# Optimization experiments

Hardware: AMD Instinct MI355X
Metric: run time of the kernel (lower is better)

The kernel has to match this reference:

```python
import jax, jax.numpy as jnp
import numpy as np

B, T, C = 8, 1024, 768
NH = 12
HD = C // NH  # 64


def setup_inputs() -> dict:
    key = jax.random.key(0)
    k1, k2, k3 = jax.random.split(key, 3)
    x = jax.random.normal(k1, (B, T, C), dtype=jnp.float32)
    w_attn = jax.random.normal(k2, (C, 3 * C), dtype=jnp.float32) * 0.02
    b_attn = jnp.zeros((3 * C,), dtype=jnp.float32)
    w_proj = jax.random.normal(k3, (C, C), dtype=jnp.float32) * 0.02
    b_proj = jnp.zeros((C,), dtype=jnp.float32)
    return {"x": x, "w_attn": w_attn, "b_attn": b_attn, "w_proj": w_proj, "b_proj": b_proj}


def reference(x, w_attn, b_attn, w_proj, b_proj):
    Bb, Tt, Cc = x.shape
    qkv = x @ w_attn + b_attn  # [B,T,3C]
    q, k, v = jnp.split(qkv, [Cc, 2 * Cc], axis=-1)
    # [B, NH, T, HD]
    q = q.reshape(Bb, Tt, NH, HD).swapaxes(1, 2)
    k = k.reshape(Bb, Tt, NH, HD).swapaxes(1, 2)
    v = v.reshape(Bb, Tt, NH, HD).swapaxes(1, 2)
    scale = 1.0 / jnp.sqrt(jnp.asarray(HD, dtype=x.dtype))
    att = jnp.einsum("bhqd,bhkd->bhqk", q, k) * scale  # [B,NH,T,T]
    causal = jnp.tril(jnp.ones((Tt, Tt), dtype=bool))[None, None]
    att = jnp.where(causal, att, jnp.asarray(-jnp.inf, dtype=att.dtype))
    att = jax.nn.softmax(att, axis=-1)
    y = jnp.einsum("bhqk,bhkd->bhqd", att, v)  # [B,NH,T,HD]
    y = y.swapaxes(1, 2).reshape(Bb, Tt, Cc)
    return y @ w_proj + b_proj
```

## Files before the change

### kernel.cpp

```cpp
#include <hip/hip_runtime.h>
#include <cstdint>
#include <cstddef>

typedef __attribute__((ext_vector_type(8))) short short8;
typedef __attribute__((ext_vector_type(4))) float f32x4;
typedef __attribute__((ext_vector_type(4))) unsigned short u16x4;
typedef __attribute__((ext_vector_type(4))) float float4v;

#define ASYNC16(gp, lp) \
  __builtin_amdgcn_global_load_lds((const __attribute__((address_space(1))) unsigned int*)(gp), \
                                   (__attribute__((address_space(3))) unsigned int*)(lp), 16, 0, 0)

__device__ __forceinline__ unsigned short f2b(float f) {
  union { float f; unsigned int u; } c; c.f = f;
  unsigned int u = c.u;
  return (unsigned short)((u + 0x7fffu + ((u >> 16) & 1u)) >> 16);
}


__global__ __launch_bounds__(256) void prep(
    const float* __restrict__ x, unsigned short* __restrict__ xb,
    const float* __restrict__ w_attn, unsigned short* __restrict__ waT,
    const float* __restrict__ w_proj, unsigned short* __restrict__ wpT) {
  __shared__ unsigned short Ts[64][65];
  const int bb = blockIdx.x;
  const int tid = threadIdx.x;
  if (bb < 3072) {
    int i = (bb * 256 + tid) * 8;
    const float* px = x + i;
    short8 v;
    for (int e = 0; e < 8; ++e) ((unsigned short*)&v)[e] = f2b(px[e]);
    *(short8*)(xb + i) = v;
    return;
  }
  const float* W; unsigned short* WT; int Kd, Nd, n0, k0;
  if (bb < 3504) {
    int t = bb - 3072; W = w_attn; WT = waT; Kd = 768; Nd = 2304;
    n0 = (t % 36) * 64; k0 = (t / 36) * 64;
  } else {
    int t = bb - 3504; W = w_proj; WT = wpT; Kd = 768; Nd = 768;
    n0 = (t % 12) * 64; k0 = (t / 12) * 64;
  }
  for (int idx = tid; idx < 4096; idx += 256) {
    int lr = idx >> 6, lc = idx & 63;
    Ts[lr][lc] = f2b(W[(size_t)(k0 + lr) * Nd + n0 + lc]);
  }
  __syncthreads();
  for (int idx = tid; idx < 4096; idx += 256) {
    int nr = idx >> 6, kc = idx & 63;
    WT[(size_t)(n0 + nr) * Kd + k0 + kc] = Ts[kc][nr];
  }
}


__global__ __launch_bounds__(256, 2) void gemm_qkv(
    const unsigned short* __restrict__ A,
    const unsigned short* __restrict__ Bt,
    const float* __restrict__ bias,
    unsigned short* __restrict__ q,
    unsigned short* __restrict__ k,
    unsigned short* __restrict__ vT)
{
  __shared__ unsigned short As[128 * 32];
  __shared__ unsigned short Bs[128 * 32];
  const int tid = threadIdx.x;
  const int w = tid >> 6, lane = tid & 63;
  const int wm = w >> 1, wn = w & 1;
  const int lr = lane & 15, lq = lane >> 4;
  const int m0 = blockIdx.x * 128, n0 = blockIdx.y * 128;
  const f32x4 fzero = {0.f, 0.f, 0.f, 0.f};

  f32x4 acc[4][4];
  for (int i = 0; i < 4; ++i) for (int j = 0; j < 4; ++j) acc[i][j] = fzero;

  for (int kk0 = 0; kk0 < 768; kk0 += 32) {
    __syncthreads();
    for (int c = 0; c < 2; ++c) {
      int base = (c * 4 + w) * 1024;
      int e = (base >> 1) + lane * 8;
      int row = e >> 5, kc = e & 31;
      ASYNC16(A  + (size_t)(m0 + row) * 768 + kk0 + kc, (char*)As + base);
      ASYNC16(Bt + (size_t)(n0 + row) * 768 + kk0 + kc, (char*)Bs + base);
    }
    __builtin_amdgcn_s_waitcnt(0);
    __syncthreads();

    short8 a[4], b[4];
    for (int i = 0; i < 4; ++i)
      a[i] = *(const short8*)(As + (wm * 64 + i * 16 + lr) * 32 + lq * 8);
    for (int j = 0; j < 4; ++j)
      b[j] = *(const short8*)(Bs + (wn * 64 + j * 16 + lr) * 32 + lq * 8);
    for (int i = 0; i < 4; ++i)
      for (int j = 0; j < 4; ++j)
        acc[i][j] = __builtin_amdgcn_mfma_f32_16x16x32_bf16(a[i], b[j], acc[i][j], 0, 0, 0);
  }

  const int colbase = n0 + wn * 64;
  const int sec = colbase / 768;
  const float QSCALE = 0.18033688011112042f;
  for (int j = 0; j < 4; ++j) {
    int col = colbase + j * 16 + lr;
    int cc = col - sec * 768;
    int h = cc >> 6, d = cc & 63;
    float bv = bias[col];
    for (int i = 0; i < 4; ++i) {
      int row0 = m0 + wm * 64 + i * 16 + lq * 4;
      int bidx = row0 >> 10, t0 = row0 & 1023;
      int bh = bidx * 12 + h;
      if (sec == 0) {
        for (int r = 0; r < 4; ++r)
          q[((size_t)bh * 1024 + t0 + r) * 64 + d] = f2b((acc[i][j][r] + bv) * QSCALE);
      } else if (sec == 1) {
        for (int r = 0; r < 4; ++r)
          k[((size_t)bh * 1024 + t0 + r) * 64 + d] = f2b(acc[i][j][r] + bv);
      } else {
        u16x4 pv;
        pv[0] = f2b(acc[i][j][0] + bv);
        pv[1] = f2b(acc[i][j][1] + bv);
        pv[2] = f2b(acc[i][j][2] + bv);
        pv[3] = f2b(acc[i][j][3] + bv);
        *(u16x4*)(vT + ((size_t)bh * 64 + d) * 1024 + t0) = pv;
      }
    }
  }
}


__global__ __launch_bounds__(256, 2) void attn(
    const unsigned short* __restrict__ q,
    const unsigned short* __restrict__ kk,
    const unsigned short* __restrict__ vT,
    unsigned short* __restrict__ y)
{
  __shared__ unsigned short Qs[64 * 72];
  __shared__ unsigned short Ks[64 * 72];
  __shared__ unsigned short Vt[64 * 72];
  __shared__ unsigned short Ps[4 * 16 * 72];

  const int tid = threadIdx.x;
  const int w = tid >> 6, lane = tid & 63;
  const int lr = lane & 15, lq = lane >> 4;
  const int g = blockIdx.x;
  const int bh = g % 96;
  const int qp = g / 96;
  const int b = bh / 12, h = bh - b * 12;
  const f32x4 fzero = {0.f, 0.f, 0.f, 0.f};

  unsigned short* Pw = Ps + w * 16 * 72;
  const unsigned short* kbase = kk + (size_t)bh * 65536;
  const unsigned short* vbase = vT + (size_t)bh * 65536;

  const int c0 = tid, c1 = tid + 256;
  short8 kreg[2], vreg[2];

  for (int half = 0; half < 2; ++half) {
    const int qt = half ? (15 - qp) : qp;
    const int q0 = qt * 64;

    __syncthreads();
    {
      const unsigned short* qptr = q + ((size_t)bh * 1024 + q0) * 64;
      short8 q0r = *(const short8*)(qptr + (size_t)c0 * 8);
      short8 q1r = *(const short8*)(qptr + (size_t)c1 * 8);
      *(short8*)(Qs + (c0 >> 3) * 72 + (c0 & 7) * 8) = q0r;
      *(short8*)(Qs + (c1 >> 3) * 72 + (c1 & 7) * 8) = q1r;
    }
    kreg[0] = *(const short8*)(kbase + (size_t)c0 * 8);
    kreg[1] = *(const short8*)(kbase + (size_t)c1 * 8);
    vreg[0] = *(const short8*)(vbase + (size_t)(c0 >> 3) * 1024 + (c0 & 7) * 8);
    vreg[1] = *(const short8*)(vbase + (size_t)(c1 >> 3) * 1024 + (c1 & 7) * 8);

    f32x4 o[4];
    float l_s[4];
    for (int jd = 0; jd < 4; ++jd) o[jd] = fzero;
    for (int r = 0; r < 4; ++r) l_s[r] = 0.0f;

    for (int kt = 0; kt <= qt; ++kt) {
      __syncthreads();
      *(short8*)(Ks + (c0 >> 3) * 72 + (c0 & 7) * 8) = kreg[0];
      *(short8*)(Ks + (c1 >> 3) * 72 + (c1 & 7) * 8) = kreg[1];
      *(short8*)(Vt + (c0 >> 3) * 72 + (c0 & 7) * 8) = vreg[0];
      *(short8*)(Vt + (c1 >> 3) * 72 + (c1 & 7) * 8) = vreg[1];
      __syncthreads();
      if (kt < qt) {
        const unsigned short* kp = kbase + (size_t)(kt + 1) * 4096;
        const unsigned short* vp = vbase + (size_t)(kt + 1) * 64;
        kreg[0] = *(const short8*)(kp + (size_t)c0 * 8);
        kreg[1] = *(const short8*)(kp + (size_t)c1 * 8);
        vreg[0] = *(const short8*)(vp + (size_t)(c0 >> 3) * 1024 + (c0 & 7) * 8);
        vreg[1] = *(const short8*)(vp + (size_t)(c1 >> 3) * 1024 + (c1 & 7) * 8);
      }

      f32x4 s[4];
      for (int j = 0; j < 4; ++j) s[j] = fzero;
      for (int ks = 0; ks < 2; ++ks) {
        short8 aq = *(const short8*)(Qs + (w * 16 + lr) * 72 + ks * 32 + lq * 8);
        short8 bk[4];
        for (int j = 0; j < 4; ++j)
          bk[j] = *(const short8*)(Ks + (j * 16 + lr) * 72 + ks * 32 + lq * 8);
        for (int j = 0; j < 4; ++j)
          s[j] = __builtin_amdgcn_mfma_f32_16x16x32_bf16(aq, bk[j], s[j], 0, 0, 0);
      }
      if (kt == qt) {
        int rowt = w * 16 + lq * 4;
        for (int j = 0; j < 4; ++j) {
          int colt = j * 16 + lr;
          for (int r = 0; r < 4; ++r)
            if (colt > rowt + r) s[j][r] = -1e30f;
        }
      }
      for (int r = 0; r < 4; ++r) {
        int prow = (lq * 4 + r) * 72;
        float acc = 0.0f;
        for (int j = 0; j < 4; ++j) {
          float p = __builtin_amdgcn_exp2f(s[j][r]);
          acc += p;
          union { float f; unsigned int u; } cv; cv.f = p;
          Pw[prow + j * 16 + lr] = (unsigned short)((cv.u + 0x8000u) >> 16);
        }
        l_s[r] += acc;
      }
      for (int ks = 0; ks < 2; ++ks) {
        short8 ap = *(const short8*)(Pw + lr * 72 + ks * 32 + lq * 8);
        short8 bv[4];
        for (int jd = 0; jd < 4; ++jd)
          bv[jd] = *(const short8*)(Vt + (jd * 16 + lr) * 72 + ks * 32 + lq * 8);
        for (int jd = 0; jd < 4; ++jd)
          o[jd] = __builtin_amdgcn_mfma_f32_16x16x32_bf16(ap, bv[jd], o[jd], 0, 0, 0);
      }
    }

    for (int r = 0; r < 4; ++r) {
      float lv = l_s[r];
      for (int off = 1; off < 16; off <<= 1)
        lv += __shfl_xor(lv, off, 16);
      l_s[r] = 1.0f / lv;
    }
    int t = q0 + w * 16 + lq * 4;
    for (int jd = 0; jd < 4; ++jd) {
      int d = jd * 16 + lr;
      for (int r = 0; r < 4; ++r)
        y[((size_t)b * 1024 + t + r) * 768 + h * 64 + d] = f2b(o[jd][r] * l_s[r]);
    }
  }
}


__global__ __launch_bounds__(256, 2) void gemm_proj(
    const unsigned short* __restrict__ A,
    const unsigned short* __restrict__ Bt,
    const float* __restrict__ bias,
    float* __restrict__ out)
{
  __shared__ unsigned short As[128 * 32];
  __shared__ unsigned short Bs[128 * 32];
  const int tid = threadIdx.x;
  const int w = tid >> 6, lane = tid & 63;
  const int wm = w >> 1, wn = w & 1;
  const int lr = lane & 15, lq = lane >> 4;
  const int m0 = blockIdx.x * 128, n0 = blockIdx.y * 128;
  const f32x4 fzero = {0.f, 0.f, 0.f, 0.f};

  f32x4 acc[4][4];
  for (int i = 0; i < 4; ++i) for (int j = 0; j < 4; ++j) acc[i][j] = fzero;

  for (int kk0 = 0; kk0 < 768; kk0 += 32) {
    __syncthreads();
    for (int c = 0; c < 2; ++c) {
      int base = (c * 4 + w) * 1024;
      int e = (base >> 1) + lane * 8;
      int row = e >> 5, kc = e & 31;
      ASYNC16(A  + (size_t)(m0 + row) * 768 + kk0 + kc, (char*)As + base);
      ASYNC16(Bt + (size_t)(n0 + row) * 768 + kk0 + kc, (char*)Bs + base);
    }
    __builtin_amdgcn_s_waitcnt(0);
    __syncthreads();

    short8 a[4], b[4];
    for (int i = 0; i < 4; ++i)
      a[i] = *(const short8*)(As + (wm * 64 + i * 16 + lr) * 32 + lq * 8);
    for (int j = 0; j < 4; ++j)
      b[j] = *(const short8*)(Bs + (wn * 64 + j * 16 + lr) * 32 + lq * 8);
    for (int i = 0; i < 4; ++i)
      for (int j = 0; j < 4; ++j)
        acc[i][j] = __builtin_amdgcn_mfma_f32_16x16x32_bf16(a[i], b[j], acc[i][j], 0, 0, 0);
  }

  for (int j = 0; j < 4; ++j) {
    int col = n0 + wn * 64 + j * 16 + lr;
    float bv = bias[col];
    for (int i = 0; i < 4; ++i) {
      int row0 = m0 + wm * 64 + i * 16 + lq * 4;
      for (int r = 0; r < 4; ++r)
        out[(size_t)(row0 + r) * 768 + col] = acc[i][j][r] + bv;
    }
  }
}


extern "C" void kernel_launch(void* const* d_in, const int* in_sizes, int n_in,
                              void* d_out, int out_size, void* d_ws, size_t ws_size,
                              hipStream_t stream) {
  const float* x      = (const float*)d_in[0];
  const float* w_attn = (const float*)d_in[1];
  const float* b_attn = (const float*)d_in[2];
  const float* w_proj = (const float*)d_in[3];
  const float* b_proj = (const float*)d_in[4];
  float* out = (float*)d_out;

  char* p = (char*)d_ws;
  unsigned short* xb  = (unsigned short*)p; p += (size_t)8192 * 768 * 2;
  unsigned short* waT = (unsigned short*)p; p += (size_t)2304 * 768 * 2;
  unsigned short* wpT = (unsigned short*)p; p += (size_t)768 * 768 * 2;
  unsigned short* qb  = (unsigned short*)p; p += (size_t)96 * 1024 * 64 * 2;
  unsigned short* kb  = (unsigned short*)p; p += (size_t)96 * 1024 * 64 * 2;
  unsigned short* vTb = (unsigned short*)p; p += (size_t)96 * 64 * 1024 * 2;
  unsigned short* yb  = (unsigned short*)p; p += (size_t)8192 * 768 * 2;

  prep<<<3648, 256, 0, stream>>>(x, xb, w_attn, waT, w_proj, wpT);
  gemm_qkv<<<dim3(64, 18), 256, 0, stream>>>(xb, waT, b_attn, qb, kb, vTb);
  attn<<<768, 256, 0, stream>>>(qb, kb, vTb, yb);
  gemm_proj<<<dim3(64, 6), 256, 0, stream>>>(yb, wpT, b_proj, out);
}
```

Before: 189.0 us.

## Process paired causal query tiles in one K/V sweep; shrink proj GEMM M-tile

The attention kernel now keeps both paired query tiles (qp and 15-qp) in shared memory and computes both in a single loop over K/V tiles. Each K/V tile is staged once, and the tile for the shorter query is skipped past its diagonal. This removes the redundant K/V loads and barriers of the second pass, at the cost of doubled accumulator registers under a tighter launch bound. The projection GEMM uses 64-row tiles with twice the grid to improve CU occupancy and tail balance.

```diff
diff --git a/kernel.cpp b/kernel.cpp
--- a/kernel.cpp
+++ b/kernel.cpp
@@ -5,7 +5,6 @@
 typedef __attribute__((ext_vector_type(8))) short short8;
 typedef __attribute__((ext_vector_type(4))) float f32x4;
 typedef __attribute__((ext_vector_type(4))) unsigned short u16x4;
-typedef __attribute__((ext_vector_type(4))) float float4v;
 
 #define ASYNC16(gp, lp) \
   __builtin_amdgcn_global_load_lds((const __attribute__((address_space(1))) unsigned int*)(gp), \
@@ -126,13 +125,13 @@
 }
 
 
-__global__ __launch_bounds__(256, 2) void attn(
+__global__ __launch_bounds__(256, 3) void attn(
     const unsigned short* __restrict__ q,
     const unsigned short* __restrict__ kk,
     const unsigned short* __restrict__ vT,
     unsigned short* __restrict__ y)
 {
-  __shared__ unsigned short Qs[64 * 72];
+  __shared__ unsigned short Qs[128 * 72];
   __shared__ unsigned short Ks[64 * 72];
   __shared__ unsigned short Vt[64 * 72];
   __shared__ unsigned short Ps[4 * 16 * 72];
@@ -143,6 +142,7 @@
   const int g = blockIdx.x;
   const int bh = g % 96;
   const int qp = g / 96;
+  const int qt1 = 15 - qp;
   const int b = bh / 12, h = bh - b * 12;
   const f32x4 fzero = {0.f, 0.f, 0.f, 0.f};
 
@@ -150,58 +150,60 @@
   const unsigned short* kbase = kk + (size_t)bh * 65536;
   const unsigned short* vbase = vT + (size_t)bh * 65536;
 
+  {
+    const unsigned short* qa = q + ((size_t)bh * 1024 + qp * 64) * 64;
+    const unsigned short* qb = q + ((size_t)bh * 1024 + qt1 * 64) * 64;
+    for (int c = tid; c < 512; c += 256) {
+      int row = c >> 3, d0 = (c & 7) * 8;
+      *(short8*)(Qs + row * 72 + d0)        = *(const short8*)(qa + (size_t)c * 8);
+      *(short8*)(Qs + (row + 64) * 72 + d0) = *(const short8*)(qb + (size_t)c * 8);
+    }
+  }
+
   const int c0 = tid, c1 = tid + 256;
   short8 kreg[2], vreg[2];
-
-  for (int half = 0; half < 2; ++half) {
-    const int qt = half ? (15 - qp) : qp;
-    const int q0 = qt * 64;
-
-    __syncthreads();
-    {
-      const unsigned short* qptr = q + ((size_t)bh * 1024 + q0) * 64;
-      short8 q0r = *(const short8*)(qptr + (size_t)c0 * 8);
-      short8 q1r = *(const short8*)(qptr + (size_t)c1 * 8);
-      *(short8*)(Qs + (c0 >> 3) * 72 + (c0 & 7) * 8) = q0r;
-      *(short8*)(Qs + (c1 >> 3) * 72 + (c1 & 7) * 8) = q1r;
-    }
-    kreg[0] = *(const short8*)(kbase + (size_t)c0 * 8);
-    kreg[1] = *(const short8*)(kbase + (size_t)c1 * 8);
-    vreg[0] = *(const short8*)(vbase + (size_t)(c0 >> 3) * 1024 + (c0 & 7) * 8);
-    vreg[1] = *(const short8*)(vbase + (size_t)(c1 >> 3) * 1024 + (c1 & 7) * 8);
-
-    f32x4 o[4];
-    float l_s[4];
-    for (int jd = 0; jd < 4; ++jd) o[jd] = fzero;
-    for (int r = 0; r < 4; ++r) l_s[r] = 0.0f;
-
-    for (int kt = 0; kt <= qt; ++kt) {
-      __syncthreads();
-      *(short8*)(Ks + (c0 >> 3) * 72 + (c0 & 7) * 8) = kreg[0];
-      *(short8*)(Ks + (c1 >> 3) * 72 + (c1 & 7) * 8) = kreg[1];
-      *(short8*)(Vt + (c0 >> 3) * 72 + (c0 & 7) * 8) = vreg[0];
-      *(short8*)(Vt + (c1 >> 3) * 72 + (c1 & 7) * 8) = vreg[1];
-      __syncthreads();
-      if (kt < qt) {
-        const unsigned short* kp = kbase + (size_t)(kt + 1) * 4096;
-        const unsigned short* vp = vbase + (size_t)(kt + 1) * 64;
-        kreg[0] = *(const short8*)(kp + (size_t)c0 * 8);
-        kreg[1] = *(const short8*)(kp + (size_t)c1 * 8);
-        vreg[0] = *(const short8*)(vp + (size_t)(c0 >> 3) * 1024 + (c0 & 7) * 8);
-        vreg[1] = *(const short8*)(vp + (size_t)(c1 >> 3) * 1024 + (c1 & 7) * 8);
-      }
-
+  kreg[0] = *(const short8*)(kbase + (size_t)c0 * 8);
+  kreg[1] = *(const short8*)(kbase + (size_t)c1 * 8);
+  vreg[0] = *(const short8*)(vbase + (size_t)(c0 >> 3) * 1024 + (c0 & 7) * 8);
+  vreg[1] = *(const short8*)(vbase + (size_t)(c1 >> 3) * 1024 + (c1 & 7) * 8);
+
+  f32x4 o0[4], o1[4];
+  float l0[4], l1[4];
+  for (int jd = 0; jd < 4; ++jd) { o0[jd] = fzero; o1[jd] = fzero; }
+  for (int r = 0; r < 4; ++r) { l0[r] = 0.0f; l1[r] = 0.0f; }
+
+  const int nkt = qt1 + 1;
+
+  for (int kt = 0; kt < nkt; ++kt) {
+    __syncthreads();
+    *(short8*)(Ks + (c0 >> 3) * 72 + (c0 & 7) * 8) = kreg[0];
+    *(short8*)(Ks + (c1 >> 3) * 72 + (c1 & 7) * 8) = kreg[1];
+    *(short8*)(Vt + (c0 >> 3) * 72 + (c0 & 7) * 8) = vreg[0];
+    *(short8*)(Vt + (c1 >> 3) * 72 + (c1 & 7) * 8) = vreg[1];
+    __syncthreads();
+    if (kt + 1 < nkt) {
+      const unsigned short* kp = kbase + (size_t)(kt + 1) * 4096;
+      const unsigned short* vp = vbase + (size_t)(kt + 1) * 64;
+      kreg[0] = *(const short8*)(kp + (size_t)c0 * 8);
+      kreg[1] = *(const short8*)(kp + (size_t)c1 * 8);
+      vreg[0] = *(const short8*)(vp + (size_t)(c0 >> 3) * 1024 + (c0 & 7) * 8);
+      vreg[1] = *(const short8*)(vp + (size_t)(c1 >> 3) * 1024 + (c1 & 7) * 8);
+    }
+
+    short8 bk[2][4];
+    for (int ks = 0; ks < 2; ++ks)
+      for (int j = 0; j < 4; ++j)
+        bk[ks][j] = *(const short8*)(Ks + (j * 16 + lr) * 72 + ks * 32 + lq * 8);
+
+    if (kt <= qp) {
       f32x4 s[4];
       for (int j = 0; j < 4; ++j) s[j] = fzero;
       for (int ks = 0; ks < 2; ++ks) {
         short8 aq = *(const short8*)(Qs + (w * 16 + lr) * 72 + ks * 32 + lq * 8);
-        short8 bk[4];
         for (int j = 0; j < 4; ++j)
-          bk[j] = *(const short8*)(Ks + (j * 16 + lr) * 72 + ks * 32 + lq * 8);
-        for (int j = 0; j < 4; ++j)
-          s[j] = __builtin_amdgcn_mfma_f32_16x16x32_bf16(aq, bk[j], s[j], 0, 0, 0);
-      }
-      if (kt == qt) {
+          s[j] = __builtin_amdgcn_mfma_f32_16x16x32_bf16(aq, bk[ks][j], s[j], 0, 0, 0);
+      }
+      if (kt == qp) {
         int rowt = w * 16 + lq * 4;
         for (int j = 0; j < 4; ++j) {
           int colt = j * 16 + lr;
@@ -218,7 +220,7 @@
           union { float f; unsigned int u; } cv; cv.f = p;
           Pw[prow + j * 16 + lr] = (unsigned short)((cv.u + 0x8000u) >> 16);
         }
-        l_s[r] += acc;
+        l0[r] += acc;
       }
       for (int ks = 0; ks < 2; ++ks) {
         short8 ap = *(const short8*)(Pw + lr * 72 + ks * 32 + lq * 8);
@@ -226,62 +228,110 @@
         for (int jd = 0; jd < 4; ++jd)
           bv[jd] = *(const short8*)(Vt + (jd * 16 + lr) * 72 + ks * 32 + lq * 8);
         for (int jd = 0; jd < 4; ++jd)
-          o[jd] = __builtin_amdgcn_mfma_f32_16x16x32_bf16(ap, bv[jd], o[jd], 0, 0, 0);
-      }
-    }
-
+          o0[jd] = __builtin_amdgcn_mfma_f32_16x16x32_bf16(ap, bv[jd], o0[jd], 0, 0, 0);
+      }
+    }
+
+    {
+      f32x4 s[4];
+      for (int j = 0; j < 4; ++j) s[j] = fzero;
+      for (int ks = 0; ks < 2; ++ks) {
+        short8 aq = *(const short8*)(Qs + (64 + w * 16 + lr) * 72 + ks * 32 + lq * 8);
+        for (int j = 0; j < 4; ++j)
+          s[j] = __builtin_amdgcn_mfma_f32_16x16x32_bf16(aq, bk[ks][j], s[j], 0, 0, 0);
+      }
+      if (kt == qt1) {
+        int rowt = w * 16 + lq * 4;
+        for (int j = 0; j < 4; ++j) {
+          int colt = j * 16 + lr;
+          for (int r = 0; r < 4; ++r)
+            if (colt > rowt + r) s[j][r] = -1e30f;
+        }
+      }
+      for (int r = 0; r < 4; ++r) {
+        int prow = (lq * 4 + r) * 72;
+        float acc = 0.0f;
+        for (int j = 0; j < 4; ++j) {
+          float p = __builtin_amdgcn_exp2f(s[j][r]);
+          acc += p;
+          union { float f; unsigned int u; } cv; cv.f = p;
+          Pw[prow + j * 16 + lr] = (unsigned short)((cv.u + 0x8000u) >> 16);
+        }
+        l1[r] += acc;
+      }
+      for (int ks = 0; ks < 2; ++ks) {
+        short8 ap = *(const short8*)(Pw + lr * 72 + ks * 32 + lq * 8);
+        short8 bv[4];
+        for (int jd = 0; jd < 4; ++jd)
+          bv[jd] = *(const short8*)(Vt + (jd * 16 + lr) * 72 + ks * 32 + lq * 8);
+        for (int jd = 0; jd < 4; ++jd)
+          o1[jd] = __builtin_amdgcn_mfma_f32_16x16x32_bf16(ap, bv[jd], o1[jd], 0, 0, 0);
+      }
+    }
+  }
+
+  for (int r = 0; r < 4; ++r) {
+    float a0 = l0[r], a1 = l1[r];
+    for (int off = 1; off < 16; off <<= 1) {
+      a0 += __shfl_xor(a0, off, 16);
+      a1 += __shfl_xor(a1, off, 16);
+    }
+    l0[r] = 1.0f / a0;
+    l1[r] = 1.0f / a1;
+  }
+  int t0 = qp * 64 + w * 16 + lq * 4;
+  int t1 = qt1 * 64 + w * 16 + lq * 4;
+  for (int jd = 0; jd < 4; ++jd) {
+    int d = jd * 16 + lr;
     for (int r = 0; r < 4; ++r) {
-      float lv = l_s[r];
-      for (int off = 1; off < 16; off <<= 1)
-        lv += __shfl_xor(lv, off, 16);
-      l_s[r] = 1.0f / lv;
-    }
-    int t = q0 + w * 16 + lq * 4;
-    for (int jd = 0; jd < 4; ++jd) {
-      int d = jd * 16 + lr;
-      for (int r = 0; r < 4; ++r)
-        y[((size_t)b * 1024 + t + r) * 768 + h * 64 + d] = f2b(o[jd][r] * l_s[r]);
-    }
-  }
-}
-
-
-__global__ __launch_bounds__(256, 2) void gemm_proj(
+      y[((size_t)b * 1024 + t0 + r) * 768 + h * 64 + d] = f2b(o0[jd][r] * l0[r]);
+      y[((size_t)b * 1024 + t1 + r) * 768 + h * 64 + d] = f2b(o1[jd][r] * l1[r]);
+    }
+  }
+}
+
+
+__global__ __launch_bounds__(256, 3) void gemm_proj(
     const unsigned short* __restrict__ A,
     const unsigned short* __restrict__ Bt,
     const float* __restrict__ bias,
     float* __restrict__ out)
 {
-  __shared__ unsigned short As[128 * 32];
+  __shared__ unsigned short As[64 * 32];
   __shared__ unsigned short Bs[128 * 32];
   const int tid = threadIdx.x;
   const int w = tid >> 6, lane = tid & 63;
   const int wm = w >> 1, wn = w & 1;
   const int lr = lane & 15, lq = lane >> 4;
-  const int m0 = blockIdx.x * 128, n0 = blockIdx.y * 128;
+  const int m0 = blockIdx.x * 64, n0 = blockIdx.y * 128;
   const f32x4 fzero = {0.f, 0.f, 0.f, 0.f};
 
-  f32x4 acc[4][4];
-  for (int i = 0; i < 4; ++i) for (int j = 0; j < 4; ++j) acc[i][j] = fzero;
+  f32x4 acc[2][4];
+  for (int i = 0; i < 2; ++i) for (int j = 0; j < 4; ++j) acc[i][j] = fzero;
+
+  const int ea = (w * 1024 >> 1) + lane * 8;
+  const int arow = ea >> 5, akc = ea & 31;
+  int sbase[2], srow[2], skc[2];
+  for (int c = 0; c < 2; ++c) {
+    sbase[c] = (c * 4 + w) * 1024;
+    int e = (sbase[c] >> 1) + lane * 8;
+    srow[c] = e >> 5; skc[c] = e & 31;
+  }
 
   for (int kk0 = 0; kk0 < 768; kk0 += 32) {
     __syncthreads();
-    for (int c = 0; c < 2; ++c) {
-      int base = (c * 4 + w) * 1024;
-      int e = (base >> 1) + lane * 8;
-      int row = e >> 5, kc = e & 31;
-      ASYNC16(A  + (size_t)(m0 + row) * 768 + kk0 + kc, (char*)As + base);
-      ASYNC16(Bt + (size_t)(n0 + row) * 768 + kk0 + kc, (char*)Bs + base);
-    }
+    ASYNC16(A + (size_t)(m0 + arow) * 768 + kk0 + akc, (char*)As + w * 1024);
+    for (int c = 0; c < 2; ++c)
+      ASYNC16(Bt + (size_t)(n0 + srow[c]) * 768 + kk0 + skc[c], (char*)Bs + sbase[c]);
     __builtin_amdgcn_s_waitcnt(0);
     __syncthreads();
 
-    short8 a[4], b[4];
-    for (int i = 0; i < 4; ++i)
-      a[i] = *(const short8*)(As + (wm * 64 + i * 16 + lr) * 32 + lq * 8);
+    short8 a[2], b[4];
+    for (int i = 0; i < 2; ++i)
+      a[i] = *(const short8*)(As + (wm * 32 + i * 16 + lr) * 32 + lq * 8);
     for (int j = 0; j < 4; ++j)
       b[j] = *(const short8*)(Bs + (wn * 64 + j * 16 + lr) * 32 + lq * 8);
-    for (int i = 0; i < 4; ++i)
+    for (int i = 0; i < 2; ++i)
       for (int j = 0; j < 4; ++j)
         acc[i][j] = __builtin_amdgcn_mfma_f32_16x16x32_bf16(a[i], b[j], acc[i][j], 0, 0, 0);
   }
@@ -289,8 +339,8 @@
   for (int j = 0; j < 4; ++j) {
     int col = n0 + wn * 64 + j * 16 + lr;
     float bv = bias[col];
-    for (int i = 0; i < 4; ++i) {
-      int row0 = m0 + wm * 64 + i * 16 + lq * 4;
+    for (int i = 0; i < 2; ++i) {
+      int row0 = m0 + wm * 32 + i * 16 + lq * 4;
       for (int r = 0; r < 4; ++r)
         out[(size_t)(row0 + r) * 768 + col] = acc[i][j][r] + bv;
     }
@@ -320,5 +370,5 @@
   prep<<<3648, 256, 0, stream>>>(x, xb, w_attn, waT, w_proj, wpT);
   gemm_qkv<<<dim3(64, 18), 256, 0, stream>>>(xb, waT, b_attn, qb, kb, vTb);
   attn<<<768, 256, 0, stream>>>(qb, kb, vTb, yb);
-  gemm_proj<<<dim3(64, 6), 256, 0, stream>>>(yb, wpT, b_proj, out);
-}
+  gemm_proj<<<dim3(128, 6), 256, 0, stream>>>(yb, wpT, b_proj, out);
+}
```

Measured after the change: 188.5 us. About the same (-0.3%).
